# Kernel tuning notes

Hardware: AMD Instinct MI355X
Metric: run time of the kernel (lower is better)

The kernel has to match this reference:

```python
import jax, jax.numpy as jnp
import numpy as np

N, E, D = 100000, 1600000, 64
L = 3          # num_layers
EPS = 1e-5     # LayerNorm eps


def setup_inputs() -> dict:
    key = jax.random.key(0)
    ks = jax.random.split(key, 8)
    s = 0.05
    return {
        "x": jax.random.normal(ks[0], (N, D), jnp.float32),
        "edge_src": jax.random.randint(ks[1], (E,), 0, N, jnp.int32),
        "edge_dst": jax.random.randint(ks[2], (E,), 0, N, jnp.int32),
        # SAGEConv: lin_l (on aggregated neighbors, with bias), lin_r (root, no bias)
        "w_l": (jax.random.normal(ks[3], (L, D, D)) * s).astype(jnp.float32),
        "b_l": jnp.zeros((L, D), jnp.float32),
        "w_r": (jax.random.normal(ks[4], (L, D, D)) * s).astype(jnp.float32),
        # LayerNorm affine params per layer
        "gamma": jnp.ones((L, D), jnp.float32),
        "beta": jnp.zeros((L, D), jnp.float32),
        # residual projection (layer 0 only; Identity afterwards)
        "w_res": (jax.random.normal(ks[5], (D, D)) * s).astype(jnp.float32),
        "b_res": jnp.zeros((D,), jnp.float32),
        # final fc
        "w_fc": (jax.random.normal(ks[6], (D, D)) * s).astype(jnp.float32),
        "b_fc": jnp.zeros((D,), jnp.float32),
    }


def _layer_norm(h, g, b):
    mu = jnp.mean(h, axis=-1, keepdims=True)
    var = jnp.var(h, axis=-1, keepdims=True)
    return (h - mu) * jax.lax.rsqrt(var + EPS) * g + b


def reference(x, edge_src, edge_dst, w_l, b_l, w_r, gamma, beta, w_res, b_res, w_fc, b_fc):
    n = x.shape[0]
    # in-degree for mean aggregation (nodes with no in-edges get 0 aggregate)
    deg = jax.ops.segment_sum(jnp.ones(edge_dst.shape, x.dtype), edge_dst, num_segments=n)
    inv_deg = jnp.where(deg > 0, 1.0 / jnp.maximum(deg, 1.0), 0.0)[:, None]  # [N,1]
    for i in range(L):
        residual = x @ w_res + b_res if i == 0 else x
        # SAGEConv mean aggregation: gather source feats, scatter-sum at dst, divide by degree
        agg = jax.ops.segment_sum(x[edge_src], edge_dst, num_segments=n) * inv_deg  # [N,D]
        h = agg @ w_l[i] + b_l[i] + x @ w_r[i]
        h = jax.nn.relu(_layer_norm(h, gamma[i], beta[i]))
        # dropout is inactive in eval mode
        x = h + residual
    return x @ w_fc + b_fc
```

## Files before the change

### kernel.cpp

```cpp
#include <hip/hip_runtime.h>

typedef unsigned short u16;
typedef __bf16 bf16x8 __attribute__((ext_vector_type(8)));
typedef float f32x4 __attribute__((ext_vector_type(4)));

#define D 64
#define LPITCH 136
#define CHUNKS 256
#define BSHIFT 9
#define CCAP 1280

__device__ __forceinline__ float b2f(u16 u) {
    unsigned v = ((unsigned)u) << 16;
    float f;
    __builtin_memcpy(&f, &v, 4);
    return f;
}
__device__ __forceinline__ float u2f_lo(unsigned u) {
    unsigned v = u << 16;
    float f;
    __builtin_memcpy(&f, &v, 4);
    return f;
}
__device__ __forceinline__ float u2f_hi(unsigned u) {
    unsigned v = u & 0xFFFF0000u;
    float f;
    __builtin_memcpy(&f, &v, 4);
    return f;
}
__device__ __forceinline__ u16 f2b(float f) {
    unsigned u;
    __builtin_memcpy(&u, &f, 4);
    u = u + 0x7FFFu + ((u >> 16) & 1u);
    return (u16)(u >> 16);
}
__device__ __forceinline__ bf16x8 ld_frag(const u16* p) {
    union { uint4 u; bf16x8 b; } cv;
    cv.u = *(const uint4*)p;
    return cv.b;
}

__global__ __launch_bounds__(256) void binA_kernel(const int* __restrict__ dst, int E,
                                                   int* __restrict__ H, int nbuck, int eper,
                                                   const float* __restrict__ xf,
                                                   u16* __restrict__ xb, int total4,
                                                   const float* __restrict__ wl,
                                                   const float* __restrict__ wr,
                                                   const float* __restrict__ wres,
                                                   const float* __restrict__ wfc,
                                                   u16* __restrict__ WtL,
                                                   u16* __restrict__ WresT,
                                                   u16* __restrict__ WfcT,
                                                   int* __restrict__ row_ptr, int N) {
    __shared__ int hist[256];
    int t = threadIdx.x;
    int c = blockIdx.x;
    hist[t] = 0;
    __syncthreads();
    {
        int beg = c * eper, end = min(beg + eper, E);
        for (int i = beg + t; i < end; i += 256)
            atomicAdd(&hist[dst[i] >> BSHIFT], 1);
    }
    __syncthreads();
    if (t < nbuck) H[c * nbuck + t] = hist[t];

    int gid = c * 256 + t;
    int gstr = CHUNKS * 256;
    if (gid == 0) row_ptr[N] = E;
    for (int i = gid; i < total4; i += gstr) {
        float4 v = *(const float4*)(xf + i * 4);
        ushort4 o;
        o.x = f2b(v.x); o.y = f2b(v.y); o.z = f2b(v.z); o.w = f2b(v.w);
        *(ushort4*)(xb + i * 4) = o;
    }
    for (int idx = gid; idx < 3 * 64 * 128; idx += gstr) {
        int l = idx >> 13;
        int rem = idx & 8191;
        int n = rem >> 7;
        int k = rem & 127;
        float v = (k < 64) ? wl[l * 4096 + k * 64 + n] : wr[l * 4096 + (k - 64) * 64 + n];
        WtL[idx] = f2b(v);
    }
    for (int idx = gid; idx < 4096; idx += gstr) {
        int n = idx >> 6, k = idx & 63;
        WresT[idx] = f2b(wres[k * 64 + n]);
        WfcT[idx] = f2b(wfc[k * 64 + n]);
    }
}

__global__ __launch_bounds__(256) void binS2_kernel(const int* __restrict__ H,
                                                    int* __restrict__ Orel,
                                                    int* __restrict__ T,
                                                    int nbuck) {
    __shared__ int ss[256];
    int b = blockIdx.x;
    int t = threadIdx.x;
    int h = H[t * nbuck + b];
    ss[t] = h;
    __syncthreads();
    for (int off = 1; off < 256; off <<= 1) {
        int v = (t >= off) ? ss[t - off] : 0;
        __syncthreads();
        ss[t] += v;
        __syncthreads();
    }
    Orel[t * nbuck + b] = ss[t] - h;
    if (t == 255) T[b] = ss[255];
}

__global__ __launch_bounds__(256) void binB_kernel(const int* __restrict__ src,
                                                   const int* __restrict__ dst, int E,
                                                   const int* __restrict__ T,
                                                   const int* __restrict__ Orel,
                                                   int* __restrict__ staging,
                                                   int nbuck, int eper) {
    __shared__ int sc[256];
    int t = threadIdx.x;
    int c = blockIdx.x;
    int v = (t < nbuck) ? T[t] : 0;
    sc[t] = v;
    __syncthreads();
    for (int off = 1; off < 256; off <<= 1) {
        int u = (t >= off) ? sc[t - off] : 0;
        __syncthreads();
        sc[t] += u;
        __syncthreads();
    }
    int baseT = sc[t] - v;
    int porel = (t < nbuck) ? Orel[c * nbuck + t] : 0;
    __syncthreads();
    sc[t] = baseT + porel;
    __syncthreads();
    int beg = c * eper, end = min(beg + eper, E);
    const int mask = (1 << BSHIFT) - 1;
    for (int i = beg + t; i < end; i += 256) {
        int d = dst[i];
        int b = d >> BSHIFT;
        int p = atomicAdd(&sc[b], 1);
        staging[p] = src[i] | ((d & mask) << 17);
    }
}

__global__ __launch_bounds__(256) void binC_kernel(const int* __restrict__ staging,
                                                   const int* __restrict__ T,
                                                   int* __restrict__ row_ptr,
                                                   float* __restrict__ inv_deg,
                                                   int* __restrict__ col, int N, int nbuck) {
    __shared__ int cnt[512];
    __shared__ int lrp[512];
    __shared__ int sm[256];
    __shared__ int span[2];
    int b = blockIdx.x;
    int t = threadIdx.x;
    int v = (t < nbuck) ? T[t] : 0;
    sm[t] = v;
    __syncthreads();
    for (int off = 1; off < 256; off <<= 1) {
        int u = (t >= off) ? sm[t - off] : 0;
        __syncthreads();
        sm[t] += u;
        __syncthreads();
    }
    if (t == b) { span[0] = sm[t] - v; span[1] = sm[t]; }
    cnt[t] = 0;
    cnt[t + 256] = 0;
    __syncthreads();
    int sbeg = span[0], send = span[1];
    int node0 = b << BSHIFT;
    int nn = min(1 << BSHIFT, N - node0);
    for (int i = sbeg + t; i < send; i += 256)
        atomicAdd(&cnt[staging[i] >> 17], 1);
    __syncthreads();
    int c0 = cnt[2 * t], c1 = cnt[2 * t + 1];
    sm[t] = c0 + c1;
    __syncthreads();
    for (int off = 1; off < 256; off <<= 1) {
        int u = (t >= off) ? sm[t - off] : 0;
        __syncthreads();
        sm[t] += u;
        __syncthreads();
    }
    int excl = sm[t] - c0 - c1;
    lrp[2 * t] = excl;
    lrp[2 * t + 1] = excl + c0;
    __syncthreads();
    for (int i = t; i < nn; i += 256) {
        row_ptr[node0 + i] = sbeg + lrp[i];
        int dd = cnt[i];
        inv_deg[node0 + i] = dd > 0 ? 1.0f / (float)dd : 0.0f;
    }
    __syncthreads();
    for (int i = sbeg + t; i < send; i += 256) {
        int word = staging[i];
        int ld = word >> 17;
        int k = atomicSub(&cnt[ld], 1) - 1;
        col[sbeg + lrp[ld] + k] = word & 0x1FFFF;
    }
}

__global__ __launch_bounds__(256, 4) void layer_kernel(const u16* __restrict__ xb_in,
                                                       const int* __restrict__ row_ptr,
                                                       const int* __restrict__ col,
                                                       const float* __restrict__ inv_deg,
                                                       const u16* __restrict__ Wt,
                                                       const float* __restrict__ bl,
                                                       const float* __restrict__ gam,
                                                       const float* __restrict__ bet,
                                                       const u16* __restrict__ WresT,
                                                       const float* __restrict__ bres,
                                                       const u16* __restrict__ WfcT,
                                                       const float* __restrict__ bfc,
                                                       u16* __restrict__ xb_out,
                                                       float* __restrict__ fout,
                                                       int N, int layer0, int final_) {
    __shared__ __align__(16) u16 sA[64 * LPITCH];
    __shared__ __align__(16) u16 sB[64 * LPITCH];
    __shared__ int lcol[CCAP];
    __shared__ int rp[65];
    __shared__ float ideg[64];
    int tid = threadIdx.x;
    int base = blockIdx.x * 64;
    int lane = tid & 63;
    int w = tid >> 6;

#pragma unroll
    for (int i = 0; i < 4; i++) {
        int idx = i * 256 + tid;
        int r = idx >> 4, c = idx & 15;
        *(uint4*)&sB[r * LPITCH + c * 8] = *(const uint4*)(Wt + idx * 8);
    }
#pragma unroll
    for (int i = 0; i < 2; i++) {
        int idx = i * 256 + tid;
        int r = idx >> 3, c = idx & 7;
        int node = base + r;
        uint4 v = make_uint4(0, 0, 0, 0);
        if (node < N) v = *(const uint4*)(xb_in + node * D + c * 8);
        *(uint4*)&sA[r * LPITCH + 64 + c * 8] = v;
    }
    if (tid < 65) rp[tid] = row_ptr[min(base + tid, N)];
    if (tid < 64) ideg[tid] = (base + tid < N) ? inv_deg[base + tid] : 0.f;
    __syncthreads();

    int e0 = rp[0];
    int tileE = rp[64] - e0;
    bool fits = tileE <= CCAP;
    if (fits) {
        for (int i = tid; i < tileE; i += 256) lcol[i] = col[e0 + i];
    }
    __syncthreads();

    int slot = lane >> 3;
    int chunk = lane & 7;
    auto run_gather = [&](auto LD) {
#pragma unroll
        for (int r = 0; r < 2; r++) {
            int node_l = w * 16 + r * 8 + slot;
            float a0 = 0, a1 = 0, a2 = 0, a3 = 0, a4 = 0, a5 = 0, a6 = 0, a7 = 0;
            int e = rp[node_l], end = rp[node_l + 1];
#define ACC(v)                                          \
    a0 += u2f_lo(v.x); a1 += u2f_hi(v.x);               \
    a2 += u2f_lo(v.y); a3 += u2f_hi(v.y);               \
    a4 += u2f_lo(v.z); a5 += u2f_hi(v.z);               \
    a6 += u2f_lo(v.w); a7 += u2f_hi(v.w);
            for (; e + 7 < end; e += 8) {
                int s0 = LD(e),     s1 = LD(e + 1), s2 = LD(e + 2), s3 = LD(e + 3);
                int s4 = LD(e + 4), s5 = LD(e + 5), s6 = LD(e + 6), s7 = LD(e + 7);
                uint4 v0 = *(const uint4*)(xb_in + s0 * D + chunk * 8);
                uint4 v1 = *(const uint4*)(xb_in + s1 * D + chunk * 8);
                uint4 v2 = *(const uint4*)(xb_in + s2 * D + chunk * 8);
                uint4 v3 = *(const uint4*)(xb_in + s3 * D + chunk * 8);
                uint4 v4 = *(const uint4*)(xb_in + s4 * D + chunk * 8);
                uint4 v5 = *(const uint4*)(xb_in + s5 * D + chunk * 8);
                uint4 v6 = *(const uint4*)(xb_in + s6 * D + chunk * 8);
                uint4 v7 = *(const uint4*)(xb_in + s7 * D + chunk * 8);
                ACC(v0) ACC(v1) ACC(v2) ACC(v3)
                ACC(v4) ACC(v5) ACC(v6) ACC(v7)
            }
            if (e + 3 < end) {
                int s0 = LD(e), s1 = LD(e + 1), s2 = LD(e + 2), s3 = LD(e + 3);
                uint4 v0 = *(const uint4*)(xb_in + s0 * D + chunk * 8);
                uint4 v1 = *(const uint4*)(xb_in + s1 * D + chunk * 8);
                uint4 v2 = *(const uint4*)(xb_in + s2 * D + chunk * 8);
                uint4 v3 = *(const uint4*)(xb_in + s3 * D + chunk * 8);
                ACC(v0) ACC(v1) ACC(v2) ACC(v3)
                e += 4;
            }
            if (e + 1 < end) {
                int s0 = LD(e), s1 = LD(e + 1);
                uint4 v0 = *(const uint4*)(xb_in + s0 * D + chunk * 8);
                uint4 v1 = *(const uint4*)(xb_in + s1 * D + chunk * 8);
                ACC(v0) ACC(v1)
                e += 2;
            }
            if (e < end) {
                int s0 = LD(e);
                uint4 v0 = *(const uint4*)(xb_in + s0 * D + chunk * 8);
                ACC(v0)
            }
#undef ACC
            float m = ideg[node_l];
            uint4 o;
            o.x = (unsigned)f2b(a0 * m) | ((unsigned)f2b(a1 * m) << 16);
            o.y = (unsigned)f2b(a2 * m) | ((unsigned)f2b(a3 * m) << 16);
            o.z = (unsigned)f2b(a4 * m) | ((unsigned)f2b(a5 * m) << 16);
            o.w = (unsigned)f2b(a6 * m) | ((unsigned)f2b(a7 * m) << 16);
            *(uint4*)&sA[node_l * LPITCH + chunk * 8] = o;
        }
    };
    if (fits) run_gather([&](int e) { return lcol[e - e0]; });
    else      run_gather([&](int e) { return col[e]; });
    __syncthreads();

    int q = lane >> 4;
    int ln = lane & 15;
    f32x4 acc[4] = {{0, 0, 0, 0}, {0, 0, 0, 0}, {0, 0, 0, 0}, {0, 0, 0, 0}};
    f32x4 accr[4] = {{0, 0, 0, 0}, {0, 0, 0, 0}, {0, 0, 0, 0}, {0, 0, 0, 0}};
    const u16* aRow = &sA[(w * 16 + ln) * LPITCH];

#pragma unroll
    for (int c = 0; c < 4; c++) {
        bf16x8 a = ld_frag(&aRow[c * 32 + q * 8]);
#pragma unroll
        for (int t = 0; t < 4; t++) {
            bf16x8 b = ld_frag(&sB[(t * 16 + ln) * LPITCH + c * 32 + q * 8]);
            acc[t] = __builtin_amdgcn_mfma_f32_16x16x32_bf16(a, b, acc[t], 0, 0, 0);
        }
    }
    if (layer0) {
#pragma unroll
        for (int c = 0; c < 2; c++) {
            bf16x8 a = ld_frag(&aRow[64 + c * 32 + q * 8]);
#pragma unroll
            for (int t = 0; t < 4; t++) {
                bf16x8 b = ld_frag(WresT + (t * 16 + ln) * 64 + c * 32 + q * 8);
                accr[t] = __builtin_amdgcn_mfma_f32_16x16x32_bf16(a, b, accr[t], 0, 0, 0);
            }
        }
    }

    float bcol[4], gcol[4], btcol[4], brcol[4];
#pragma unroll
    for (int t = 0; t < 4; t++) {
        int colI = t * 16 + ln;
        bcol[t] = bl[colI];
        gcol[t] = gam[colI];
        btcol[t] = bet[colI];
        brcol[t] = layer0 ? bres[colI] : 0.f;
    }
#pragma unroll
    for (int t = 0; t < 4; t++)
#pragma unroll
        for (int r = 0; r < 4; r++) acc[t][r] += bcol[t];

    float ps[4], pq[4];
#pragma unroll
    for (int r = 0; r < 4; r++) {
        float s = 0, s2 = 0;
#pragma unroll
        for (int t = 0; t < 4; t++) { float h = acc[t][r]; s += h; s2 += h * h; }
        ps[r] = s; pq[r] = s2;
    }
    for (int off = 1; off < 16; off <<= 1) {
#pragma unroll
        for (int r = 0; r < 4; r++) {
            ps[r] += __shfl_xor(ps[r], off, 64);
            pq[r] += __shfl_xor(pq[r], off, 64);
        }
    }
#pragma unroll
    for (int r = 0; r < 4; r++) {
        int nb = w * 16 + q * 4 + r;
        float mu = ps[r] * (1.f / 64.f);
        float var = pq[r] * (1.f / 64.f) - mu * mu;
        var = var < 0.f ? 0.f : var;
        float rstd = rsqrtf(var + 1e-5f);
#pragma unroll
        for (int t = 0; t < 4; t++) {
            int colI = t * 16 + ln;
            float hn = (acc[t][r] - mu) * rstd * gcol[t] + btcol[t];
            hn = hn > 0.f ? hn : 0.f;
            float res = layer0 ? (accr[t][r] + brcol[t])
                               : b2f(sA[nb * LPITCH + 64 + colI]);
            sA[nb * LPITCH + colI] = f2b(hn + res);
        }
    }

    if (final_) {
        f32x4 accf[4] = {{0, 0, 0, 0}, {0, 0, 0, 0}, {0, 0, 0, 0}, {0, 0, 0, 0}};
#pragma unroll
        for (int c = 0; c < 2; c++) {
            bf16x8 a = ld_frag(&aRow[c * 32 + q * 8]);
#pragma unroll
            for (int t = 0; t < 4; t++) {
                bf16x8 b = ld_frag(WfcT + (t * 16 + ln) * 64 + c * 32 + q * 8);
                accf[t] = __builtin_amdgcn_mfma_f32_16x16x32_bf16(a, b, accf[t], 0, 0, 0);
            }
        }
        __syncthreads();
        float* fB = (float*)sB;
#pragma unroll
        for (int r = 0; r < 4; r++) {
            int nb = w * 16 + q * 4 + r;
#pragma unroll
            for (int t = 0; t < 4; t++) {
                int colI = t * 16 + ln;
                fB[nb * 68 + colI] = accf[t][r] + bfc[colI];
            }
        }
        __syncthreads();
#pragma unroll
        for (int i = 0; i < 4; i++) {
            int idx = i * 256 + tid;
            int row = idx >> 4, cc = idx & 15;
            int node = base + row;
            if (node < N)
                *(float4*)(fout + node * D + cc * 4) = *(const float4*)&fB[row * 68 + cc * 4];
        }
    } else {
#pragma unroll
        for (int i = 0; i < 2; i++) {
            int idx = i * 64 + lane;
            int row = w * 16 + (idx >> 3);
            int ch = idx & 7;
            int node = base + row;
            if (node < N)
                *(uint4*)(xb_out + node * D + ch * 8) = *(const uint4*)&sA[row * LPITCH + ch * 8];
        }
    }
}

extern "C" void kernel_launch(void* const* d_in, const int* in_sizes, int n_in,
                              void* d_out, int out_size, void* d_ws, size_t ws_size,
                              hipStream_t stream) {
    const float* x_in = (const float*)d_in[0];
    const int* e_src = (const int*)d_in[1];
    const int* e_dst = (const int*)d_in[2];
    const float* w_l = (const float*)d_in[3];
    const float* b_l = (const float*)d_in[4];
    const float* w_r = (const float*)d_in[5];
    const float* gam = (const float*)d_in[6];
    const float* bet = (const float*)d_in[7];
    const float* w_res = (const float*)d_in[8];
    const float* b_res = (const float*)d_in[9];
    const float* w_fc = (const float*)d_in[10];
    const float* b_fc = (const float*)d_in[11];
    float* out = (float*)d_out;

    const int N = in_sizes[0] / D;
    const int E = in_sizes[1];
    const int nbuck = ((N - 1) >> BSHIFT) + 1;
    const int eper = (E + CHUNKS - 1) / CHUNKS;

    size_t o = 0;
    auto carve = [&](size_t bytes) {
        size_t cur = o;
        o += (bytes + 255) & ~(size_t)255;
        return (char*)d_ws + cur;
    };
    int* row_ptr = (int*)carve((size_t)(N + 1) * 4);
    float* inv_deg = (float*)carve((size_t)N * 4);
    int* colA = (int*)carve((size_t)E * 4);
    int* staging = (int*)carve((size_t)E * 4);
    int* Hh = (int*)carve((size_t)CHUNKS * nbuck * 4);
    int* Orel = (int*)carve((size_t)CHUNKS * nbuck * 4);
    int* Tb = (int*)carve((size_t)nbuck * 4);
    u16* WtL = (u16*)carve(3 * 64 * 128 * 2);
    u16* WresT = (u16*)carve(64 * 64 * 2);
    u16* WfcT = (u16*)carve(64 * 64 * 2);
    u16* xbA = (u16*)carve((size_t)N * D * 2);
    u16* xbB = (u16*)carve((size_t)N * D * 2);

    binA_kernel<<<CHUNKS, 256, 0, stream>>>(e_dst, E, Hh, nbuck, eper,
                                            x_in, xbA, N * D / 4,
                                            w_l, w_r, w_res, w_fc, WtL, WresT, WfcT,
                                            row_ptr, N);
    binS2_kernel<<<nbuck, 256, 0, stream>>>(Hh, Orel, Tb, nbuck);
    binB_kernel<<<CHUNKS, 256, 0, stream>>>(e_src, e_dst, E, Tb, Orel, staging,
                                            nbuck, eper);
    binC_kernel<<<nbuck, 256, 0, stream>>>(staging, Tb, row_ptr, inv_deg, colA, N, nbuck);

    int gridT = (N + 63) / 64;

    layer_kernel<<<gridT, 256, 0, stream>>>(xbA, row_ptr, colA, inv_deg, WtL,
                                            b_l, gam, bet, WresT, b_res,
                                            WfcT, b_fc, xbB, out, N, 1, 0);
    layer_kernel<<<gridT, 256, 0, stream>>>(xbB, row_ptr, colA, inv_deg, WtL + 8192,
                                            b_l + 64, gam + 64, bet + 64, WresT, b_res,
                                            WfcT, b_fc, xbA, out, N, 0, 0);
    layer_kernel<<<gridT, 256, 0, stream>>>(xbA, row_ptr, colA, inv_deg, WtL + 16384,
                                            b_l + 128, gam + 128, bet + 128, WresT, b_res,
                                            WfcT, b_fc, xbB, out, N, 0, 1);
}
```

Before: 272.2 us.

## Replace two-level bucket sort CSR build with global-atomic degree count and scatter

Replaces the bucketed histogram/staging/local-sort CSR construction with a direct approach: global atomic degree counting, a three-kernel prefix scan over per-node degrees, and a global-atomic cursor scatter of source indices into col. This removes the staging buffer pass and per-bucket local sorting. In exchange it adds many contended global atomics and a memset, and neighbor order within a row becomes nondeterministic, which may hurt gather locality in the layer kernels.

```diff
diff --git a/kernel.cpp b/kernel.cpp
--- a/kernel.cpp
+++ b/kernel.cpp
@@ -6,9 +6,8 @@
 
 #define D 64
 #define LPITCH 136
-#define CHUNKS 256
-#define BSHIFT 9
 #define CCAP 1280
+#define PGRID 1024
 
 __device__ __forceinline__ float b2f(u16 u) {
     unsigned v = ((unsigned)u) << 16;
@@ -40,8 +39,8 @@
     return cv.b;
 }
 
-__global__ __launch_bounds__(256) void binA_kernel(const int* __restrict__ dst, int E,
-                                                   int* __restrict__ H, int nbuck, int eper,
+__global__ __launch_bounds__(256) void prep_kernel(const int* __restrict__ dst, int E,
+                                                   int* __restrict__ deg,
                                                    const float* __restrict__ xf,
                                                    u16* __restrict__ xb, int total4,
                                                    const float* __restrict__ wl,
@@ -52,22 +51,20 @@
                                                    u16* __restrict__ WresT,
                                                    u16* __restrict__ WfcT,
                                                    int* __restrict__ row_ptr, int N) {
-    __shared__ int hist[256];
-    int t = threadIdx.x;
-    int c = blockIdx.x;
-    hist[t] = 0;
-    __syncthreads();
-    {
-        int beg = c * eper, end = min(beg + eper, E);
-        for (int i = beg + t; i < end; i += 256)
-            atomicAdd(&hist[dst[i] >> BSHIFT], 1);
-    }
-    __syncthreads();
-    if (t < nbuck) H[c * nbuck + t] = hist[t];
-
-    int gid = c * 256 + t;
-    int gstr = CHUNKS * 256;
+    int gid = blockIdx.x * 256 + threadIdx.x;
+    int gstr = PGRID * 256;
     if (gid == 0) row_ptr[N] = E;
+
+    int e4 = E >> 2;
+    for (int i = gid; i < e4; i += gstr) {
+        int4 d = *(const int4*)(dst + i * 4);
+        atomicAdd(&deg[d.x], 1);
+        atomicAdd(&deg[d.y], 1);
+        atomicAdd(&deg[d.z], 1);
+        atomicAdd(&deg[d.w], 1);
+    }
+    for (int i = e4 * 4 + gid; i < E; i += gstr) atomicAdd(&deg[dst[i]], 1);
+
     for (int i = gid; i < total4; i += gstr) {
         float4 v = *(const float4*)(xf + i * 4);
         ushort4 o;
@@ -89,113 +86,117 @@
     }
 }
 
-__global__ __launch_bounds__(256) void binS2_kernel(const int* __restrict__ H,
-                                                    int* __restrict__ Orel,
-                                                    int* __restrict__ T,
-                                                    int nbuck) {
+__global__ __launch_bounds__(256) void scanA_kernel(const int* __restrict__ deg,
+                                                    int* __restrict__ bsum, int N) {
+    __shared__ int red[256];
+    int b = blockIdx.x, t = threadIdx.x;
+    int base = b * 1024 + t * 4;
+    int s = 0;
+    if (base + 3 < N) {
+        int4 v = *(const int4*)(deg + base);
+        s = v.x + v.y + v.z + v.w;
+    } else {
+        for (int k = 0; k < 4; k++)
+            if (base + k < N) s += deg[base + k];
+    }
+    red[t] = s;
+    __syncthreads();
+    for (int off = 128; off > 0; off >>= 1) {
+        if (t < off) red[t] += red[t + off];
+        __syncthreads();
+    }
+    if (t == 0) bsum[b] = red[0];
+}
+
+__global__ __launch_bounds__(256) void scanB_kernel(int* __restrict__ bsum, int nb) {
     __shared__ int ss[256];
-    int b = blockIdx.x;
     int t = threadIdx.x;
-    int h = H[t * nbuck + b];
-    ss[t] = h;
+    int v = (t < nb) ? bsum[t] : 0;
+    ss[t] = v;
     __syncthreads();
     for (int off = 1; off < 256; off <<= 1) {
-        int v = (t >= off) ? ss[t - off] : 0;
-        __syncthreads();
-        ss[t] += v;
-        __syncthreads();
-    }
-    Orel[t * nbuck + b] = ss[t] - h;
-    if (t == 255) T[b] = ss[255];
-}
-
-__global__ __launch_bounds__(256) void binB_kernel(const int* __restrict__ src,
+        int u = (t >= off) ? ss[t - off] : 0;
+        __syncthreads();
+        ss[t] += u;
+        __syncthreads();
+    }
+    if (t < nb) bsum[t] = ss[t] - v;
+}
+
+__global__ __launch_bounds__(256) void scanC_kernel(const int* __restrict__ deg,
+                                                    const int* __restrict__ bsum,
+                                                    int* __restrict__ row_ptr,
+                                                    int* __restrict__ cursor,
+                                                    float* __restrict__ inv_deg, int N) {
+    __shared__ int ss[256];
+    int b = blockIdx.x, t = threadIdx.x;
+    int base = b * 1024 + t * 4;
+    int d0 = 0, d1 = 0, d2 = 0, d3 = 0;
+    bool full = (base + 3 < N);
+    if (full) {
+        int4 v = *(const int4*)(deg + base);
+        d0 = v.x; d1 = v.y; d2 = v.z; d3 = v.w;
+    } else {
+        if (base < N) d0 = deg[base];
+        if (base + 1 < N) d1 = deg[base + 1];
+        if (base + 2 < N) d2 = deg[base + 2];
+        if (base + 3 < N) d3 = deg[base + 3];
+    }
+    int s = d0 + d1 + d2 + d3;
+    ss[t] = s;
+    __syncthreads();
+    for (int off = 1; off < 256; off <<= 1) {
+        int u = (t >= off) ? ss[t - off] : 0;
+        __syncthreads();
+        ss[t] += u;
+        __syncthreads();
+    }
+    int p0 = bsum[b] + ss[t] - s;
+    int p1 = p0 + d0, p2 = p1 + d1, p3 = p2 + d2;
+    if (full) {
+        *(int4*)(row_ptr + base) = make_int4(p0, p1, p2, p3);
+        *(int4*)(cursor + base) = make_int4(p0, p1, p2, p3);
+        float4 iv;
+        iv.x = d0 > 0 ? 1.0f / (float)d0 : 0.0f;
+        iv.y = d1 > 0 ? 1.0f / (float)d1 : 0.0f;
+        iv.z = d2 > 0 ? 1.0f / (float)d2 : 0.0f;
+        iv.w = d3 > 0 ? 1.0f / (float)d3 : 0.0f;
+        *(float4*)(inv_deg + base) = iv;
+    } else {
+        int pp[4] = {p0, p1, p2, p3};
+        int dd[4] = {d0, d1, d2, d3};
+        for (int k = 0; k < 4; k++) {
+            if (base + k < N) {
+                row_ptr[base + k] = pp[k];
+                cursor[base + k] = pp[k];
+                inv_deg[base + k] = dd[k] > 0 ? 1.0f / (float)dd[k] : 0.0f;
+            }
+        }
+    }
+}
+
+__global__ __launch_bounds__(256) void scat_kernel(const int* __restrict__ src,
                                                    const int* __restrict__ dst, int E,
-                                                   const int* __restrict__ T,
-                                                   const int* __restrict__ Orel,
-                                                   int* __restrict__ staging,
-                                                   int nbuck, int eper) {
-    __shared__ int sc[256];
-    int t = threadIdx.x;
-    int c = blockIdx.x;
-    int v = (t < nbuck) ? T[t] : 0;
-    sc[t] = v;
-    __syncthreads();
-    for (int off = 1; off < 256; off <<= 1) {
-        int u = (t >= off) ? sc[t - off] : 0;
-        __syncthreads();
-        sc[t] += u;
-        __syncthreads();
-    }
-    int baseT = sc[t] - v;
-    int porel = (t < nbuck) ? Orel[c * nbuck + t] : 0;
-    __syncthreads();
-    sc[t] = baseT + porel;
-    __syncthreads();
-    int beg = c * eper, end = min(beg + eper, E);
-    const int mask = (1 << BSHIFT) - 1;
-    for (int i = beg + t; i < end; i += 256) {
-        int d = dst[i];
-        int b = d >> BSHIFT;
-        int p = atomicAdd(&sc[b], 1);
-        staging[p] = src[i] | ((d & mask) << 17);
-    }
-}
-
-__global__ __launch_bounds__(256) void binC_kernel(const int* __restrict__ staging,
-                                                   const int* __restrict__ T,
-                                                   int* __restrict__ row_ptr,
-                                                   float* __restrict__ inv_deg,
-                                                   int* __restrict__ col, int N, int nbuck) {
-    __shared__ int cnt[512];
-    __shared__ int lrp[512];
-    __shared__ int sm[256];
-    __shared__ int span[2];
-    int b = blockIdx.x;
-    int t = threadIdx.x;
-    int v = (t < nbuck) ? T[t] : 0;
-    sm[t] = v;
-    __syncthreads();
-    for (int off = 1; off < 256; off <<= 1) {
-        int u = (t >= off) ? sm[t - off] : 0;
-        __syncthreads();
-        sm[t] += u;
-        __syncthreads();
-    }
-    if (t == b) { span[0] = sm[t] - v; span[1] = sm[t]; }
-    cnt[t] = 0;
-    cnt[t + 256] = 0;
-    __syncthreads();
-    int sbeg = span[0], send = span[1];
-    int node0 = b << BSHIFT;
-    int nn = min(1 << BSHIFT, N - node0);
-    for (int i = sbeg + t; i < send; i += 256)
-        atomicAdd(&cnt[staging[i] >> 17], 1);
-    __syncthreads();
-    int c0 = cnt[2 * t], c1 = cnt[2 * t + 1];
-    sm[t] = c0 + c1;
-    __syncthreads();
-    for (int off = 1; off < 256; off <<= 1) {
-        int u = (t >= off) ? sm[t - off] : 0;
-        __syncthreads();
-        sm[t] += u;
-        __syncthreads();
-    }
-    int excl = sm[t] - c0 - c1;
-    lrp[2 * t] = excl;
-    lrp[2 * t + 1] = excl + c0;
-    __syncthreads();
-    for (int i = t; i < nn; i += 256) {
-        row_ptr[node0 + i] = sbeg + lrp[i];
-        int dd = cnt[i];
-        inv_deg[node0 + i] = dd > 0 ? 1.0f / (float)dd : 0.0f;
-    }
-    __syncthreads();
-    for (int i = sbeg + t; i < send; i += 256) {
-        int word = staging[i];
-        int ld = word >> 17;
-        int k = atomicSub(&cnt[ld], 1) - 1;
-        col[sbeg + lrp[ld] + k] = word & 0x1FFFF;
+                                                   int* __restrict__ cursor,
+                                                   int* __restrict__ col) {
+    int gid = blockIdx.x * 256 + threadIdx.x;
+    int gstr = PGRID * 256;
+    int e4 = E >> 2;
+    for (int i = gid; i < e4; i += gstr) {
+        int4 s = *(const int4*)(src + i * 4);
+        int4 d = *(const int4*)(dst + i * 4);
+        int p0 = atomicAdd(&cursor[d.x], 1);
+        col[p0] = s.x;
+        int p1 = atomicAdd(&cursor[d.y], 1);
+        col[p1] = s.y;
+        int p2 = atomicAdd(&cursor[d.z], 1);
+        col[p2] = s.z;
+        int p3 = atomicAdd(&cursor[d.w], 1);
+        col[p3] = s.w;
+    }
+    for (int i = e4 * 4 + gid; i < E; i += gstr) {
+        int p = atomicAdd(&cursor[dst[i]], 1);
+        col[p] = src[i];
     }
 }
 
@@ -450,8 +451,7 @@
 
     const int N = in_sizes[0] / D;
     const int E = in_sizes[1];
-    const int nbuck = ((N - 1) >> BSHIFT) + 1;
-    const int eper = (E + CHUNKS - 1) / CHUNKS;
+    const int nb = (N + 1023) / 1024;
 
     size_t o = 0;
     auto carve = [&](size_t bytes) {
@@ -462,24 +462,24 @@
     int* row_ptr = (int*)carve((size_t)(N + 1) * 4);
     float* inv_deg = (float*)carve((size_t)N * 4);
     int* colA = (int*)carve((size_t)E * 4);
-    int* staging = (int*)carve((size_t)E * 4);
-    int* Hh = (int*)carve((size_t)CHUNKS * nbuck * 4);
-    int* Orel = (int*)carve((size_t)CHUNKS * nbuck * 4);
-    int* Tb = (int*)carve((size_t)nbuck * 4);
+    int* deg = (int*)carve((size_t)N * 4);
+    int* cursor = (int*)carve((size_t)N * 4);
+    int* bsum = (int*)carve(256 * 4);
     u16* WtL = (u16*)carve(3 * 64 * 128 * 2);
     u16* WresT = (u16*)carve(64 * 64 * 2);
     u16* WfcT = (u16*)carve(64 * 64 * 2);
     u16* xbA = (u16*)carve((size_t)N * D * 2);
     u16* xbB = (u16*)carve((size_t)N * D * 2);
 
-    binA_kernel<<<CHUNKS, 256, 0, stream>>>(e_dst, E, Hh, nbuck, eper,
-                                            x_in, xbA, N * D / 4,
-                                            w_l, w_r, w_res, w_fc, WtL, WresT, WfcT,
-                                            row_ptr, N);
-    binS2_kernel<<<nbuck, 256, 0, stream>>>(Hh, Orel, Tb, nbuck);
-    binB_kernel<<<CHUNKS, 256, 0, stream>>>(e_src, e_dst, E, Tb, Orel, staging,
-                                            nbuck, eper);
-    binC_kernel<<<nbuck, 256, 0, stream>>>(staging, Tb, row_ptr, inv_deg, colA, N, nbuck);
+    hipMemsetAsync(deg, 0, (size_t)N * 4, stream);
+    prep_kernel<<<PGRID, 256, 0, stream>>>(e_dst, E, deg,
+                                           x_in, xbA, N * D / 4,
+                                           w_l, w_r, w_res, w_fc, WtL, WresT, WfcT,
+                                           row_ptr, N);
+    scanA_kernel<<<nb, 256, 0, stream>>>(deg, bsum, N);
+    scanB_kernel<<<1, 256, 0, stream>>>(bsum, nb);
+    scanC_kernel<<<nb, 256, 0, stream>>>(deg, bsum, row_ptr, cursor, inv_deg, N);
+    scat_kernel<<<PGRID, 256, 0, stream>>>(e_src, e_dst, E, cursor, colA);
 
     int gridT = (N + 63) / 64;
 
```

Result: slower. 399.5 us (+46.8%).

## Use finer CSR buckets and more edge chunks; split conversion into own kernel

Applied to the files above, without the earlier changes.

Halves the destination bucket size (512 to 256 nodes), so there are about 391 buckets, and doubles the edge chunk count to 512. The scan kernels now process two elements per thread to cover the larger bucket and chunk counts. The x/weight bf16 conversion moves out of the histogram kernel into a separate tail kernel with its own 1024-block grid. The aim is more parallel blocks in the CSR build and less serial per-block work, at the cost of an extra launch and a larger histogram matrix.

```diff
diff --git a/kernel.cpp b/kernel.cpp
--- a/kernel.cpp
+++ b/kernel.cpp
@@ -6,9 +6,10 @@
 
 #define D 64
 #define LPITCH 136
-#define CHUNKS 256
-#define BSHIFT 9
+#define CHUNKS 512
+#define BSHIFT 8
 #define CCAP 1280
+#define TGRID 1024
 
 __device__ __forceinline__ float b2f(u16 u) {
     unsigned v = ((unsigned)u) << 16;
@@ -41,8 +42,22 @@
 }
 
 __global__ __launch_bounds__(256) void binA_kernel(const int* __restrict__ dst, int E,
-                                                   int* __restrict__ H, int nbuck, int eper,
-                                                   const float* __restrict__ xf,
+                                                   int* __restrict__ H, int nbuck,
+                                                   int eper) {
+    __shared__ int hist[512];
+    int t = threadIdx.x;
+    int c = blockIdx.x;
+    hist[t] = 0;
+    hist[t + 256] = 0;
+    __syncthreads();
+    int beg = c * eper, end = min(beg + eper, E);
+    for (int i = beg + t; i < end; i += 256)
+        atomicAdd(&hist[dst[i] >> BSHIFT], 1);
+    __syncthreads();
+    for (int b = t; b < nbuck; b += 256) H[c * nbuck + b] = hist[b];
+}
+
+__global__ __launch_bounds__(256) void tail_kernel(const float* __restrict__ xf,
                                                    u16* __restrict__ xb, int total4,
                                                    const float* __restrict__ wl,
                                                    const float* __restrict__ wr,
@@ -51,22 +66,10 @@
                                                    u16* __restrict__ WtL,
                                                    u16* __restrict__ WresT,
                                                    u16* __restrict__ WfcT,
-                                                   int* __restrict__ row_ptr, int N) {
-    __shared__ int hist[256];
-    int t = threadIdx.x;
-    int c = blockIdx.x;
-    hist[t] = 0;
-    __syncthreads();
-    {
-        int beg = c * eper, end = min(beg + eper, E);
-        for (int i = beg + t; i < end; i += 256)
-            atomicAdd(&hist[dst[i] >> BSHIFT], 1);
-    }
-    __syncthreads();
-    if (t < nbuck) H[c * nbuck + t] = hist[t];
-
-    int gid = c * 256 + t;
-    int gstr = CHUNKS * 256;
+                                                   int* __restrict__ row_ptr,
+                                                   int N, int E) {
+    int gid = blockIdx.x * 256 + threadIdx.x;
+    int gstr = TGRID * 256;
     if (gid == 0) row_ptr[N] = E;
     for (int i = gid; i < total4; i += gstr) {
         float4 v = *(const float4*)(xf + i * 4);
@@ -96,8 +99,10 @@
     __shared__ int ss[256];
     int b = blockIdx.x;
     int t = threadIdx.x;
-    int h = H[t * nbuck + b];
-    ss[t] = h;
+    int h0 = H[(2 * t) * nbuck + b];
+    int h1 = H[(2 * t + 1) * nbuck + b];
+    int s = h0 + h1;
+    ss[t] = s;
     __syncthreads();
     for (int off = 1; off < 256; off <<= 1) {
         int v = (t >= off) ? ss[t - off] : 0;
@@ -105,7 +110,9 @@
         ss[t] += v;
         __syncthreads();
     }
-    Orel[t * nbuck + b] = ss[t] - h;
+    int excl = ss[t] - s;
+    Orel[(2 * t) * nbuck + b] = excl;
+    Orel[(2 * t + 1) * nbuck + b] = excl + h0;
     if (t == 255) T[b] = ss[255];
 }
 
@@ -115,22 +122,26 @@
                                                    const int* __restrict__ Orel,
                                                    int* __restrict__ staging,
                                                    int nbuck, int eper) {
-    __shared__ int sc[256];
+    __shared__ int sc[512];
+    __shared__ int ss[256];
     int t = threadIdx.x;
     int c = blockIdx.x;
-    int v = (t < nbuck) ? T[t] : 0;
-    sc[t] = v;
+    int v0 = (2 * t < nbuck) ? T[2 * t] : 0;
+    int v1 = (2 * t + 1 < nbuck) ? T[2 * t + 1] : 0;
+    int s = v0 + v1;
+    ss[t] = s;
     __syncthreads();
     for (int off = 1; off < 256; off <<= 1) {
-        int u = (t >= off) ? sc[t - off] : 0;
-        __syncthreads();
-        sc[t] += u;
-        __syncthreads();
-    }
-    int baseT = sc[t] - v;
-    int porel = (t < nbuck) ? Orel[c * nbuck + t] : 0;
-    __syncthreads();
-    sc[t] = baseT + porel;
+        int u = (t >= off) ? ss[t - off] : 0;
+        __syncthreads();
+        ss[t] += u;
+        __syncthreads();
+    }
+    int base0 = ss[t] - s;
+    int o0 = (2 * t < nbuck) ? Orel[c * nbuck + 2 * t] : 0;
+    int o1 = (2 * t + 1 < nbuck) ? Orel[c * nbuck + 2 * t + 1] : 0;
+    sc[2 * t] = base0 + o0;
+    sc[2 * t + 1] = base0 + v0 + o1;
     __syncthreads();
     int beg = c * eper, end = min(beg + eper, E);
     const int mask = (1 << BSHIFT) - 1;
@@ -147,14 +158,16 @@
                                                    int* __restrict__ row_ptr,
                                                    float* __restrict__ inv_deg,
                                                    int* __restrict__ col, int N, int nbuck) {
-    __shared__ int cnt[512];
-    __shared__ int lrp[512];
+    __shared__ int cnt[256];
+    __shared__ int lrp[256];
     __shared__ int sm[256];
     __shared__ int span[2];
     int b = blockIdx.x;
     int t = threadIdx.x;
-    int v = (t < nbuck) ? T[t] : 0;
-    sm[t] = v;
+    int v0 = (2 * t < nbuck) ? T[2 * t] : 0;
+    int v1 = (2 * t + 1 < nbuck) ? T[2 * t + 1] : 0;
+    int s = v0 + v1;
+    sm[t] = s;
     __syncthreads();
     for (int off = 1; off < 256; off <<= 1) {
         int u = (t >= off) ? sm[t - off] : 0;
@@ -162,9 +175,10 @@
         sm[t] += u;
         __syncthreads();
     }
-    if (t == b) { span[0] = sm[t] - v; span[1] = sm[t]; }
+    int base0 = sm[t] - s;
+    if (2 * t == b)     { span[0] = base0;       span[1] = base0 + v0; }
+    if (2 * t + 1 == b) { span[0] = base0 + v0;  span[1] = base0 + v0 + v1; }
     cnt[t] = 0;
-    cnt[t + 256] = 0;
     __syncthreads();
     int sbeg = span[0], send = span[1];
     int node0 = b << BSHIFT;
@@ -172,8 +186,8 @@
     for (int i = sbeg + t; i < send; i += 256)
         atomicAdd(&cnt[staging[i] >> 17], 1);
     __syncthreads();
-    int c0 = cnt[2 * t], c1 = cnt[2 * t + 1];
-    sm[t] = c0 + c1;
+    int c0 = cnt[t];
+    sm[t] = c0;
     __syncthreads();
     for (int off = 1; off < 256; off <<= 1) {
         int u = (t >= off) ? sm[t - off] : 0;
@@ -181,14 +195,11 @@
         sm[t] += u;
         __syncthreads();
     }
-    int excl = sm[t] - c0 - c1;
-    lrp[2 * t] = excl;
-    lrp[2 * t + 1] = excl + c0;
-    __syncthreads();
-    for (int i = t; i < nn; i += 256) {
-        row_ptr[node0 + i] = sbeg + lrp[i];
-        int dd = cnt[i];
-        inv_deg[node0 + i] = dd > 0 ? 1.0f / (float)dd : 0.0f;
+    lrp[t] = sm[t] - c0;
+    __syncthreads();
+    if (t < nn) {
+        row_ptr[node0 + t] = sbeg + lrp[t];
+        inv_deg[node0 + t] = c0 > 0 ? 1.0f / (float)c0 : 0.0f;
     }
     __syncthreads();
     for (int i = sbeg + t; i < send; i += 256) {
@@ -472,10 +483,10 @@
     u16* xbA = (u16*)carve((size_t)N * D * 2);
     u16* xbB = (u16*)carve((size_t)N * D * 2);
 
-    binA_kernel<<<CHUNKS, 256, 0, stream>>>(e_dst, E, Hh, nbuck, eper,
-                                            x_in, xbA, N * D / 4,
-                                            w_l, w_r, w_res, w_fc, WtL, WresT, WfcT,
-                                            row_ptr, N);
+    binA_kernel<<<CHUNKS, 256, 0, stream>>>(e_dst, E, Hh, nbuck, eper);
+    tail_kernel<<<TGRID, 256, 0, stream>>>(x_in, xbA, N * D / 4,
+                                           w_l, w_r, w_res, w_fc, WtL, WresT, WfcT,
+                                           row_ptr, N, E);
     binS2_kernel<<<nbuck, 256, 0, stream>>>(Hh, Orel, Tb, nbuck);
     binB_kernel<<<CHUNKS, 256, 0, stream>>>(e_src, e_dst, E, Tb, Orel, staging,
                                             nbuck, eper);
```

Result: no change. 269.4 us (-1.0%).

## Fuse four CSR-building kernels into one persistent kernel with grid barriers

Applied to the files above, without the earlier changes.

Merges the histogram, per-bucket scan, scatter-to-staging and per-bucket local sort kernels into a single kernel of 256 blocks. The stages are separated by a software grid barrier built on global atomics. This removes three kernel launches and the gaps between them. In exchange the later stages use only 256 blocks instead of one block per bucket, and correctness depends on all 256 blocks being resident at the same time.

```diff
diff --git a/kernel.cpp b/kernel.cpp
--- a/kernel.cpp
+++ b/kernel.cpp
@@ -40,41 +40,59 @@
     return cv.b;
 }
 
-__global__ __launch_bounds__(256) void binA_kernel(const int* __restrict__ dst, int E,
-                                                   int* __restrict__ H, int nbuck, int eper,
-                                                   const float* __restrict__ xf,
-                                                   u16* __restrict__ xb, int total4,
-                                                   const float* __restrict__ wl,
-                                                   const float* __restrict__ wr,
-                                                   const float* __restrict__ wres,
-                                                   const float* __restrict__ wfc,
-                                                   u16* __restrict__ WtL,
-                                                   u16* __restrict__ WresT,
-                                                   u16* __restrict__ WfcT,
-                                                   int* __restrict__ row_ptr, int N) {
-    __shared__ int hist[256];
+__device__ __forceinline__ void gbar(int* bar, int nb) {
+    __threadfence();
+    __syncthreads();
+    if (threadIdx.x == 0) {
+        int g = __hip_atomic_load(bar + 1, __ATOMIC_RELAXED, __HIP_MEMORY_SCOPE_AGENT);
+        int old = __hip_atomic_fetch_add(bar, 1, __ATOMIC_RELAXED, __HIP_MEMORY_SCOPE_AGENT);
+        if (old == nb - 1) {
+            __hip_atomic_store(bar, 0, __ATOMIC_RELAXED, __HIP_MEMORY_SCOPE_AGENT);
+            __hip_atomic_fetch_add(bar + 1, 1, __ATOMIC_RELEASE, __HIP_MEMORY_SCOPE_AGENT);
+        } else {
+            while (__hip_atomic_load(bar + 1, __ATOMIC_RELAXED, __HIP_MEMORY_SCOPE_AGENT) == g)
+                __builtin_amdgcn_s_sleep(8);
+        }
+        __threadfence();
+    }
+    __syncthreads();
+}
+
+__global__ __launch_bounds__(256) void csr_fused(
+    const int* __restrict__ src, const int* __restrict__ dst, int E,
+    const float* __restrict__ xf, u16* __restrict__ xb, int total4,
+    const float* __restrict__ wl, const float* __restrict__ wr,
+    const float* __restrict__ wres, const float* __restrict__ wfc,
+    u16* __restrict__ WtL, u16* __restrict__ WresT, u16* __restrict__ WfcT,
+    int* __restrict__ H, int* __restrict__ Orel, int* __restrict__ T,
+    int* __restrict__ staging, int* __restrict__ row_ptr,
+    float* __restrict__ inv_deg, int* __restrict__ col,
+    int* __restrict__ bar, int N, int nbuck, int eper) {
+
+    __shared__ int shA[512];
+    __shared__ int shB[512];
+    __shared__ int sm[256];
+    __shared__ int tb[513];
+
     int t = threadIdx.x;
     int c = blockIdx.x;
-    hist[t] = 0;
-    __syncthreads();
-    {
-        int beg = c * eper, end = min(beg + eper, E);
-        for (int i = beg + t; i < end; i += 256)
-            atomicAdd(&hist[dst[i] >> BSHIFT], 1);
-    }
-    __syncthreads();
-    if (t < nbuck) H[c * nbuck + t] = hist[t];
-
     int gid = c * 256 + t;
-    int gstr = CHUNKS * 256;
+    int nb = gridDim.x;
+    int beg = c * eper, end = min(beg + eper, E);
+
+    shA[t] = 0;
+    shA[t + 256] = 0;
+    __syncthreads();
+    for (int i = beg + t; i < end; i += 256)
+        atomicAdd(&shA[dst[i] >> BSHIFT], 1);
     if (gid == 0) row_ptr[N] = E;
-    for (int i = gid; i < total4; i += gstr) {
+    for (int i = gid; i < total4; i += CHUNKS * 256) {
         float4 v = *(const float4*)(xf + i * 4);
         ushort4 o;
         o.x = f2b(v.x); o.y = f2b(v.y); o.z = f2b(v.z); o.w = f2b(v.w);
         *(ushort4*)(xb + i * 4) = o;
     }
-    for (int idx = gid; idx < 3 * 64 * 128; idx += gstr) {
+    for (int idx = gid; idx < 3 * 64 * 128; idx += CHUNKS * 256) {
         int l = idx >> 13;
         int rem = idx & 8191;
         int n = rem >> 7;
@@ -82,120 +100,101 @@
         float v = (k < 64) ? wl[l * 4096 + k * 64 + n] : wr[l * 4096 + (k - 64) * 64 + n];
         WtL[idx] = f2b(v);
     }
-    for (int idx = gid; idx < 4096; idx += gstr) {
+    for (int idx = gid; idx < 4096; idx += CHUNKS * 256) {
         int n = idx >> 6, k = idx & 63;
         WresT[idx] = f2b(wres[k * 64 + n]);
         WfcT[idx] = f2b(wfc[k * 64 + n]);
     }
-}
-
-__global__ __launch_bounds__(256) void binS2_kernel(const int* __restrict__ H,
-                                                    int* __restrict__ Orel,
-                                                    int* __restrict__ T,
-                                                    int nbuck) {
-    __shared__ int ss[256];
-    int b = blockIdx.x;
-    int t = threadIdx.x;
-    int h = H[t * nbuck + b];
-    ss[t] = h;
-    __syncthreads();
-    for (int off = 1; off < 256; off <<= 1) {
-        int v = (t >= off) ? ss[t - off] : 0;
-        __syncthreads();
-        ss[t] += v;
-        __syncthreads();
-    }
-    Orel[t * nbuck + b] = ss[t] - h;
-    if (t == 255) T[b] = ss[255];
-}
-
-__global__ __launch_bounds__(256) void binB_kernel(const int* __restrict__ src,
-                                                   const int* __restrict__ dst, int E,
-                                                   const int* __restrict__ T,
-                                                   const int* __restrict__ Orel,
-                                                   int* __restrict__ staging,
-                                                   int nbuck, int eper) {
-    __shared__ int sc[256];
-    int t = threadIdx.x;
-    int c = blockIdx.x;
-    int v = (t < nbuck) ? T[t] : 0;
-    sc[t] = v;
-    __syncthreads();
-    for (int off = 1; off < 256; off <<= 1) {
-        int u = (t >= off) ? sc[t - off] : 0;
-        __syncthreads();
-        sc[t] += u;
-        __syncthreads();
-    }
-    int baseT = sc[t] - v;
-    int porel = (t < nbuck) ? Orel[c * nbuck + t] : 0;
-    __syncthreads();
-    sc[t] = baseT + porel;
-    __syncthreads();
-    int beg = c * eper, end = min(beg + eper, E);
-    const int mask = (1 << BSHIFT) - 1;
-    for (int i = beg + t; i < end; i += 256) {
-        int d = dst[i];
-        int b = d >> BSHIFT;
-        int p = atomicAdd(&sc[b], 1);
-        staging[p] = src[i] | ((d & mask) << 17);
-    }
-}
-
-__global__ __launch_bounds__(256) void binC_kernel(const int* __restrict__ staging,
-                                                   const int* __restrict__ T,
-                                                   int* __restrict__ row_ptr,
-                                                   float* __restrict__ inv_deg,
-                                                   int* __restrict__ col, int N, int nbuck) {
-    __shared__ int cnt[512];
-    __shared__ int lrp[512];
-    __shared__ int sm[256];
-    __shared__ int span[2];
-    int b = blockIdx.x;
-    int t = threadIdx.x;
-    int v = (t < nbuck) ? T[t] : 0;
-    sm[t] = v;
-    __syncthreads();
-    for (int off = 1; off < 256; off <<= 1) {
-        int u = (t >= off) ? sm[t - off] : 0;
-        __syncthreads();
-        sm[t] += u;
-        __syncthreads();
-    }
-    if (t == b) { span[0] = sm[t] - v; span[1] = sm[t]; }
-    cnt[t] = 0;
-    cnt[t + 256] = 0;
-    __syncthreads();
-    int sbeg = span[0], send = span[1];
-    int node0 = b << BSHIFT;
-    int nn = min(1 << BSHIFT, N - node0);
-    for (int i = sbeg + t; i < send; i += 256)
-        atomicAdd(&cnt[staging[i] >> 17], 1);
-    __syncthreads();
-    int c0 = cnt[2 * t], c1 = cnt[2 * t + 1];
-    sm[t] = c0 + c1;
-    __syncthreads();
-    for (int off = 1; off < 256; off <<= 1) {
-        int u = (t >= off) ? sm[t - off] : 0;
-        __syncthreads();
-        sm[t] += u;
-        __syncthreads();
-    }
-    int excl = sm[t] - c0 - c1;
-    lrp[2 * t] = excl;
-    lrp[2 * t + 1] = excl + c0;
-    __syncthreads();
-    for (int i = t; i < nn; i += 256) {
-        row_ptr[node0 + i] = sbeg + lrp[i];
-        int dd = cnt[i];
-        inv_deg[node0 + i] = dd > 0 ? 1.0f / (float)dd : 0.0f;
-    }
-    __syncthreads();
-    for (int i = sbeg + t; i < send; i += 256) {
-        int word = staging[i];
-        int ld = word >> 17;
-        int k = atomicSub(&cnt[ld], 1) - 1;
-        col[sbeg + lrp[ld] + k] = word & 0x1FFFF;
+    __syncthreads();
+    for (int b = t; b < nbuck; b += 256) H[c * nbuck + b] = shA[b];
+
+    gbar(bar, nb);
+
+    for (int b = c; b < nbuck; b += nb) {
+        int h = H[t * nbuck + b];
+        sm[t] = h;
+        __syncthreads();
+        for (int off = 1; off < 256; off <<= 1) {
+            int v = (t >= off) ? sm[t - off] : 0;
+            __syncthreads();
+            sm[t] += v;
+            __syncthreads();
+        }
+        Orel[t * nbuck + b] = sm[t] - h;
+        if (t == 255) T[b] = sm[255];
+        __syncthreads();
+    }
+
+    gbar(bar, nb);
+
+    {
+        int v0 = (2 * t < nbuck) ? T[2 * t] : 0;
+        int v1 = (2 * t + 1 < nbuck) ? T[2 * t + 1] : 0;
+        int s = v0 + v1;
+        sm[t] = s;
+        __syncthreads();
+        for (int off = 1; off < 256; off <<= 1) {
+            int u = (t >= off) ? sm[t - off] : 0;
+            __syncthreads();
+            sm[t] += u;
+            __syncthreads();
+        }
+        int base0 = sm[t] - s;
+        int o0 = (2 * t < nbuck) ? Orel[c * nbuck + 2 * t] : 0;
+        int o1 = (2 * t + 1 < nbuck) ? Orel[c * nbuck + 2 * t + 1] : 0;
+        shA[2 * t] = base0 + o0;
+        shA[2 * t + 1] = base0 + v0 + o1;
+        tb[2 * t] = base0;
+        tb[2 * t + 1] = base0 + v0;
+        if (t == 255) tb[512] = sm[255];
+        __syncthreads();
+        const int mask = (1 << BSHIFT) - 1;
+        for (int i = beg + t; i < end; i += 256) {
+            int d = dst[i];
+            int b = d >> BSHIFT;
+            int p = atomicAdd(&shA[b], 1);
+            staging[p] = src[i] | ((d & mask) << 17);
+        }
+    }
+
+    gbar(bar, nb);
+
+    for (int b = c; b < nbuck; b += nb) {
+        int sbeg = tb[b], send = tb[b + 1];
+        shA[t] = 0;
+        shA[t + 256] = 0;
+        __syncthreads();
+        int node0 = b << BSHIFT;
+        int nn = min(1 << BSHIFT, N - node0);
+        for (int i = sbeg + t; i < send; i += 256)
+            atomicAdd(&shA[staging[i] >> 17], 1);
+        __syncthreads();
+        int c0 = shA[2 * t], c1 = shA[2 * t + 1];
+        sm[t] = c0 + c1;
+        __syncthreads();
+        for (int off = 1; off < 256; off <<= 1) {
+            int u = (t >= off) ? sm[t - off] : 0;
+            __syncthreads();
+            sm[t] += u;
+            __syncthreads();
+        }
+        int excl = sm[t] - c0 - c1;
+        shB[2 * t] = excl;
+        shB[2 * t + 1] = excl + c0;
+        __syncthreads();
+        for (int i = t; i < nn; i += 256) {
+            row_ptr[node0 + i] = sbeg + shB[i];
+            int dd = shA[i];
+            inv_deg[node0 + i] = dd > 0 ? 1.0f / (float)dd : 0.0f;
+        }
+        __syncthreads();
+        for (int i = sbeg + t; i < send; i += 256) {
+            int word = staging[i];
+            int ld = word >> 17;
+            int k = atomicSub(&shA[ld], 1) - 1;
+            col[sbeg + shB[ld] + k] = word & 0x1FFFF;
+        }
+        __syncthreads();
     }
 }
 
@@ -466,20 +465,20 @@
     int* Hh = (int*)carve((size_t)CHUNKS * nbuck * 4);
     int* Orel = (int*)carve((size_t)CHUNKS * nbuck * 4);
     int* Tb = (int*)carve((size_t)nbuck * 4);
+    int* bar = (int*)carve(2 * 4);
     u16* WtL = (u16*)carve(3 * 64 * 128 * 2);
     u16* WresT = (u16*)carve(64 * 64 * 2);
     u16* WfcT = (u16*)carve(64 * 64 * 2);
     u16* xbA = (u16*)carve((size_t)N * D * 2);
     u16* xbB = (u16*)carve((size_t)N * D * 2);
 
-    binA_kernel<<<CHUNKS, 256, 0, stream>>>(e_dst, E, Hh, nbuck, eper,
-                                            x_in, xbA, N * D / 4,
-                                            w_l, w_r, w_res, w_fc, WtL, WresT, WfcT,
-                                            row_ptr, N);
-    binS2_kernel<<<nbuck, 256, 0, stream>>>(Hh, Orel, Tb, nbuck);
-    binB_kernel<<<CHUNKS, 256, 0, stream>>>(e_src, e_dst, E, Tb, Orel, staging,
-                                            nbuck, eper);
-    binC_kernel<<<nbuck, 256, 0, stream>>>(staging, Tb, row_ptr, inv_deg, colA, N, nbuck);
+    hipMemsetAsync(bar, 0, 8, stream);
+    csr_fused<<<CHUNKS, 256, 0, stream>>>(e_src, e_dst, E,
+                                          x_in, xbA, N * D / 4,
+                                          w_l, w_r, w_res, w_fc, WtL, WresT, WfcT,
+                                          Hh, Orel, Tb, staging,
+                                          row_ptr, inv_deg, colA,
+                                          bar, N, nbuck, eper);
 
     int gridT = (N + 63) / 64;
 
```

After: 416.6 us. 53.1% more time.
